# Kernel optimization log

Measured on AMD Instinct MI355X. Metric: run time of the kernel, lower is better.

The kernel has to match this reference:

```python
import jax, jax.numpy as jnp
import numpy as np

B, S, D, H, E = 4, 1024, 1024, 16, 4
HD = D // H
FF = 4 * D
EPS = 1e-5


def _ln(x):
    # normalize only; per-expert affine applied by caller
    mu = jnp.mean(x, axis=-1, keepdims=True)
    var = jnp.mean(jnp.square(x - mu), axis=-1, keepdims=True)
    return (x - mu) * jax.lax.rsqrt(var + EPS)


def setup_inputs() -> dict:
    key = jax.random.key(0)
    ks = jax.random.split(key, 12)
    s = 0.02
    inp = {
        "x": jax.random.normal(ks[0], (B, S, D), jnp.float32),
        # attention router
        "Wr_a": jax.random.normal(ks[1], (D, E), jnp.float32) * s,
        "br_a": jnp.zeros((E,), jnp.float32),
        # per-expert attention params
        "g_a": jnp.ones((E, D), jnp.float32),
        "b_a": jnp.zeros((E, D), jnp.float32),
        "Wqkv": jax.random.normal(ks[2], (E, D, 3 * D), jnp.float32) * s,
        "bqkv": jnp.zeros((E, 3 * D), jnp.float32),
        "Wpr": jax.random.normal(ks[3], (E, D, D), jnp.float32) * s,
        "bpr": jnp.zeros((E, D), jnp.float32),
        # MLP router
        "Wr_m": jax.random.normal(ks[4], (D, E), jnp.float32) * s,
        "br_m": jnp.zeros((E,), jnp.float32),
        # per-expert MLP params
        "g_m": jnp.ones((E, D), jnp.float32),
        "b_m": jnp.zeros((E, D), jnp.float32),
        "Wfc": jax.random.normal(ks[5], (E, D, FF), jnp.float32) * s,
        "bfc": jnp.zeros((E, FF), jnp.float32),
        "Wp2": jax.random.normal(ks[6], (E, FF, D), jnp.float32) * s,
        "bp2": jnp.zeros((E, D), jnp.float32),
    }
    return inp


def _block(x, Wr_a, br_a, g_a, b_a, Wqkv, bqkv, Wpr, bpr,
           Wr_m, br_m, g_m, b_m, Wfc, bfc, Wp2, bp2):
    N = B * S
    h = x.reshape(N, D)

    # ---- MoT attention (routing_all_possible_path: dense score-weighted mix) ----
    score = jax.nn.softmax(h @ Wr_a + br_a, axis=-1)          # [N,E]
    hn = _ln(h)                                                # shared normalization
    hln = hn[None, :, :] * g_a[:, None, :] + b_a[:, None, :]  # [E,N,D]
    qkv_e = jnp.einsum('end,edf->enf', hln, Wqkv) + bqkv[:, None, :]  # [E,N,3D]
    qkv = jnp.einsum('ne,enf->nf', score, qkv_e)               # [N,3D]

    q, k, v = jnp.split(qkv.reshape(B, S, 3 * D), 3, axis=-1)
    q = q.reshape(B, S, H, HD).transpose(0, 2, 1, 3)           # [B,H,S,hd]
    k = k.reshape(B, S, H, HD).transpose(0, 2, 1, 3)
    v = v.reshape(B, S, H, HD).transpose(0, 2, 1, 3)

    aw = jnp.einsum('bhqd,bhkd->bhqk', q, k) / jnp.sqrt(jnp.float32(HD))
    causal = jnp.tril(jnp.ones((S, S), bool))
    aw = jnp.where(causal, aw, jnp.finfo(aw.dtype).min)
    p = jax.nn.softmax(aw, axis=-1)
    a = jnp.einsum('bhqk,bhkd->bhqd', p, v)                    # [B,H,S,hd]
    a = a.transpose(0, 2, 1, 3).reshape(N, D)

    attn_out = jnp.einsum('ne,nd,edf->nf', score, a, Wpr) + score @ bpr
    y = x + attn_out.reshape(B, S, D)

    # ---- MoT MLP (same dense routed-expert pattern) ----
    h2 = y.reshape(N, D)
    score2 = jax.nn.softmax(h2 @ Wr_m + br_m, axis=-1)         # [N,E]
    hn2 = _ln(h2)
    hln2 = hn2[None, :, :] * g_m[:, None, :] + b_m[:, None, :]  # [E,N,D]
    inter = jax.nn.gelu(jnp.einsum('end,edf->enf', hln2, Wfc) + bfc[:, None, :])  # [E,N,FF]
    mlp_out = jnp.einsum('ne,enf,efd->nd', score2, inter, Wp2) + score2 @ bp2
    return y + mlp_out.reshape(B, S, D)


def reference(x, Wr_a, br_a, g_a, b_a, Wqkv, bqkv, Wpr, bpr,
              Wr_m, br_m, g_m, b_m, Wfc, bfc, Wp2, bp2):
    return _block(x, Wr_a, br_a, g_a, b_a, Wqkv, bqkv, Wpr, bpr,
                  Wr_m, br_m, g_m, b_m, Wfc, bfc, Wp2, bp2)
```

## Files before the change

### kernel.cpp

```cpp
#include <hip/hip_runtime.h>
#include <hip/hip_bf16.h>

typedef __bf16 bf16x8 __attribute__((ext_vector_type(8)));
typedef float f32x4 __attribute__((ext_vector_type(4)));
typedef unsigned short u16;
typedef u16 u16x8 __attribute__((ext_vector_type(8)));
typedef u16 u16x4 __attribute__((ext_vector_type(4)));

#define B_ 4
#define S_ 1024
#define D_ 1024
#define E_ 4
#define H_ 16
#define FF_ 4096
#define N_ 4096

__device__ __forceinline__ u16 f2bf(float f) {
  __hip_bfloat16 h = __float2bfloat16(f);
  return *reinterpret_cast<u16*>(&h);
}
__device__ __forceinline__ float bf2f(u16 v) {
  return __uint_as_float(((unsigned)v) << 16);
}

#define BAR()                         \
  {                                   \
    asm volatile("" ::: "memory");    \
    __builtin_amdgcn_s_barrier();     \
    asm volatile("" ::: "memory");    \
  }

__global__ __launch_bounds__(256) void tcvt(const float* __restrict__ src,
                                            u16* __restrict__ dst, int R, int C) {
  __shared__ float t[32][33];
  int r0 = blockIdx.y * 32, c0 = blockIdx.x * 32;
  int tx = threadIdx.x, ty = threadIdx.y;
#pragma unroll
  for (int i = 0; i < 4; i++)
    t[ty + i * 8][tx] = src[(long)(r0 + ty + i * 8) * C + c0 + tx];
  __syncthreads();
#pragma unroll
  for (int i = 0; i < 4; i++)
    dst[(long)(c0 + ty + i * 8) * R + r0 + tx] = f2bf(t[tx][ty + i * 8]);
}

template <int YMODE>
__global__ __launch_bounds__(256) void ln_router_expand(
    const float* __restrict__ X, const float* __restrict__ Wr, const float* __restrict__ br,
    const float* __restrict__ g, const float* __restrict__ bb,
    float* __restrict__ score_out, u16* __restrict__ Aout,
    long stride_e, long stride_n, int scale_flag,
    const float* __restrict__ score_a, const float* __restrict__ bpr,
    const u16* __restrict__ prt, float* __restrict__ ybuf) {
  int n = blockIdx.x, t = threadIdx.x;
  int lane = t & 63, wave = t >> 6;
  int d0 = t * 4;
  const float* xr = X + (long)n * D_;
  float4 xv = *reinterpret_cast<const float4*>(&xr[d0]);
  if (YMODE) {
    float4 sa4 = reinterpret_cast<const float4*>(score_a)[n];
    float4 b0 = *reinterpret_cast<const float4*>(&bpr[d0]);
    float4 b1 = *reinterpret_cast<const float4*>(&bpr[D_ + d0]);
    float4 b2 = *reinterpret_cast<const float4*>(&bpr[2 * D_ + d0]);
    float4 b3 = *reinterpret_cast<const float4*>(&bpr[3 * D_ + d0]);
    xv.x += sa4.x * b0.x + sa4.y * b1.x + sa4.z * b2.x + sa4.w * b3.x;
    xv.y += sa4.x * b0.y + sa4.y * b1.y + sa4.z * b2.y + sa4.w * b3.y;
    xv.z += sa4.x * b0.z + sa4.y * b1.z + sa4.z * b2.z + sa4.w * b3.z;
    xv.w += sa4.x * b0.w + sa4.y * b1.w + sa4.z * b2.w + sa4.w * b3.w;
    long idx = (long)n * D_ + d0;
#pragma unroll
    for (int zz = 0; zz < 4; zz++) {
      u16x4 pv = *reinterpret_cast<const u16x4*>(&prt[(long)zz * 4194304 + idx]);
      xv.x += bf2f(pv[0]); xv.y += bf2f(pv[1]); xv.z += bf2f(pv[2]); xv.w += bf2f(pv[3]);
    }
    *reinterpret_cast<float4*>(&ybuf[idx]) = xv;
  }
  float vals[6];
  vals[0] = xv.x + xv.y + xv.z + xv.w;
  vals[1] = xv.x * xv.x + xv.y * xv.y + xv.z * xv.z + xv.w * xv.w;
  {
    float4 w0 = reinterpret_cast<const float4*>(Wr)[d0];
    float4 w1 = reinterpret_cast<const float4*>(Wr)[d0 + 1];
    float4 w2 = reinterpret_cast<const float4*>(Wr)[d0 + 2];
    float4 w3 = reinterpret_cast<const float4*>(Wr)[d0 + 3];
    vals[2] = xv.x * w0.x + xv.y * w1.x + xv.z * w2.x + xv.w * w3.x;
    vals[3] = xv.x * w0.y + xv.y * w1.y + xv.z * w2.y + xv.w * w3.y;
    vals[4] = xv.x * w0.z + xv.y * w1.z + xv.z * w2.z + xv.w * w3.z;
    vals[5] = xv.x * w0.w + xv.y * w1.w + xv.z * w2.w + xv.w * w3.w;
  }
#pragma unroll
  for (int o = 1; o < 64; o <<= 1) {
#pragma unroll
    for (int j = 0; j < 6; j++) vals[j] += __shfl_xor(vals[j], o, 64);
  }
  __shared__ float red[4][6];
  if (lane == 0) {
#pragma unroll
    for (int j = 0; j < 6; j++) red[wave][j] = vals[j];
  }
  __syncthreads();
  float tot[6];
#pragma unroll
  for (int j = 0; j < 6; j++) tot[j] = red[0][j] + red[1][j] + red[2][j] + red[3][j];
  float mean = tot[0] * (1.0f / D_);
  float var = tot[1] * (1.0f / D_) - mean * mean;
  float rstd = rsqrtf(var + 1e-5f);
  float lg0 = tot[2] + br[0], lg1 = tot[3] + br[1], lg2 = tot[4] + br[2], lg3 = tot[5] + br[3];
  float mx = fmaxf(fmaxf(lg0, lg1), fmaxf(lg2, lg3));
  float e0 = __expf(lg0 - mx), e1 = __expf(lg1 - mx), e2 = __expf(lg2 - mx), e3 = __expf(lg3 - mx);
  float inv = 1.0f / (e0 + e1 + e2 + e3);
  float sc[4] = {e0 * inv, e1 * inv, e2 * inv, e3 * inv};
  if (t == 0) {
    float4 s4 = make_float4(sc[0], sc[1], sc[2], sc[3]);
    *reinterpret_cast<float4*>(&score_out[(long)n * 4]) = s4;
  }
  float4 hn;
  hn.x = (xv.x - mean) * rstd; hn.y = (xv.y - mean) * rstd;
  hn.z = (xv.z - mean) * rstd; hn.w = (xv.w - mean) * rstd;
#pragma unroll
  for (int e = 0; e < 4; e++) {
    float4 ge = *reinterpret_cast<const float4*>(&g[e * D_ + d0]);
    float4 be = *reinterpret_cast<const float4*>(&bb[e * D_ + d0]);
    float s = scale_flag ? sc[e] : 1.0f;
    u16x4 o;
    o[0] = f2bf((hn.x * ge.x + be.x) * s);
    o[1] = f2bf((hn.y * ge.y + be.y) * s);
    o[2] = f2bf((hn.z * ge.z + be.z) * s);
    o[3] = f2bf((hn.w * ge.w + be.w) * s);
    *reinterpret_cast<u16x4*>(&Aout[(long)e * stride_e + (long)n * stride_n + d0]) = o;
  }
}

template <int MODE>
__global__ __launch_bounds__(512, 2) void g8(
    const u16* __restrict__ A, const u16* __restrict__ Bt, int K, int N, int kslice,
    const float* __restrict__ score, const float* __restrict__ bias,
    u16* __restrict__ outb, int eidx, long zstride) {
  __shared__ __align__(16) u16 lds0[65536];
  const int tid = threadIdx.x;
  const int w = tid >> 6, lane = tid & 63;
  const int l15 = lane & 15, l4 = lane >> 4;
  const int wr = w >> 2, wc = w & 3;

  const int gx = gridDim.x, gy = gridDim.y;
  const int total = gx * gy * gridDim.z;
  const int flat = blockIdx.x + gx * (blockIdx.y + gy * blockIdx.z);
  const int cpx = total >> 3;
  const int nf = (flat & 7) * cpx + (flat >> 3);
  const int bxi = nf % gx;
  const int tmp = nf / gx;
  const int byi = tmp % gy;
  const int z = tmp / gy;

  const long bm = (long)byi * 256, bn = (long)bxi * 256;
  const long k0 = (long)z * kslice;
  const int nt = kslice >> 6;

  const int cp = lane & 3;
  const int sr0 = w * 32 + (lane >> 2);
  const int sr1 = sr0 + 16;
  const int cl0 = cp ^ ((sr0 >> 1) & 3);
  const int cl1 = cp ^ ((sr1 >> 1) & 3);
  const u16* gA0 = A + (bm + sr0) * (long)K + k0 + cl0 * 8;
  const u16* gA1 = A + (bm + sr1) * (long)K + k0 + cl1 * 8;
  const u16* gB0 = Bt + (bn + sr0) * (long)K + k0 + cl0 * 8;
  const u16* gB1 = Bt + (bn + sr1) * (long)K + k0 + cl1 * 8;
  const int e0 = w * 1024;
  const int e1 = w * 1024 + 512;

  const int chA = l4 ^ ((l15 >> 1) & 3);
  const int rdA = (wr * 128 + l15) * 32 + chA * 8;
  const int rdB = (wc * 64 + l15) * 32 + chA * 8;

#define GLD(gsrc, ldsoff)                                                              \
  __builtin_amdgcn_global_load_lds(                                                    \
      (const __attribute__((address_space(1))) void*)(gsrc),                           \
      (__attribute__((address_space(3))) void*)(lds0 + (ldsoff)), 16, 0, 0)

  GLD(gA0, 0 + e0);
  GLD(gA1, 0 + e1);
  GLD(gB0, 16384 + e0);
  GLD(gB1, 16384 + e1);
  GLD(gA0 + 32, 8192 + e0);
  GLD(gA1 + 32, 8192 + e1);
  GLD(gB0 + 32, 24576 + e0);
  GLD(gB1 + 32, 24576 + e1);
  if (nt > 1) {
    GLD(gA0 + 64, 32768 + e0);
    GLD(gA1 + 64, 32768 + e1);
    GLD(gB0 + 64, 32768 + 16384 + e0);
    GLD(gB1 + 64, 32768 + 16384 + e1);
    asm volatile("s_waitcnt vmcnt(8)" ::: "memory");
  } else {
    asm volatile("s_waitcnt vmcnt(4)" ::: "memory");
  }
  BAR();

  f32x4 acc[8][4] = {};
  bf16x8 a[8], b[4];

  for (int t = 0; t < nt; ++t) {
    const int base = (t & 1) * 32768;
    const int nb = base ^ 32768;
    const long ko1 = (long)(t + 1) * 64 + 32;
    const long ko2 = (long)(t + 2) * 64;
#pragma unroll
    for (int i = 0; i < 8; i++) a[i] = *(const bf16x8*)(lds0 + base + rdA + i * 512);
#pragma unroll
    for (int i = 0; i < 4; i++) b[i] = *(const bf16x8*)(lds0 + base + 16384 + rdB + i * 512);
    if (t + 1 < nt) {
      GLD(gA0 + ko1, nb + 8192 + e0);
      GLD(gA1 + ko1, nb + 8192 + e1);
      GLD(gB0 + ko1, nb + 24576 + e0);
      GLD(gB1 + ko1, nb + 24576 + e1);
    }
    BAR();
    __builtin_amdgcn_s_setprio(1);
#pragma unroll
    for (int mi = 0; mi < 8; mi++)
#pragma unroll
      for (int ni = 0; ni < 4; ni++)
        acc[mi][ni] = __builtin_amdgcn_mfma_f32_16x16x32_bf16(a[mi], b[ni], acc[mi][ni], 0, 0, 0);
    __builtin_amdgcn_s_setprio(0);
    if (t + 1 < nt) {
      asm volatile("s_waitcnt vmcnt(8)" ::: "memory");
    } else {
      asm volatile("s_waitcnt vmcnt(0)" ::: "memory");
    }
    BAR();
#pragma unroll
    for (int i = 0; i < 8; i++) a[i] = *(const bf16x8*)(lds0 + base + 8192 + rdA + i * 512);
#pragma unroll
    for (int i = 0; i < 4; i++) b[i] = *(const bf16x8*)(lds0 + base + 24576 + rdB + i * 512);
    if (t + 2 < nt) {
      GLD(gA0 + ko2, base + e0);
      GLD(gA1 + ko2, base + e1);
      GLD(gB0 + ko2, base + 16384 + e0);
      GLD(gB1 + ko2, base + 16384 + e1);
    }
    BAR();
    __builtin_amdgcn_s_setprio(1);
#pragma unroll
    for (int mi = 0; mi < 8; mi++)
#pragma unroll
      for (int ni = 0; ni < 4; ni++)
        acc[mi][ni] = __builtin_amdgcn_mfma_f32_16x16x32_bf16(a[mi], b[ni], acc[mi][ni], 0, 0, 0);
    __builtin_amdgcn_s_setprio(0);
    if (t + 2 < nt) {
      asm volatile("s_waitcnt vmcnt(8)" ::: "memory");
    } else if (t + 1 < nt) {
      asm volatile("s_waitcnt vmcnt(4)" ::: "memory");
    } else {
      asm volatile("s_waitcnt vmcnt(0)" ::: "memory");
    }
    BAR();
  }
#undef GLD

  const long zoff = (long)z * zstride;
#pragma unroll
  for (int ni = 0; ni < 4; ni++) {
    long col = bn + wc * 64 + ni * 16 + l15;
    float b4[4];
    float bcol = 0.0f;
    if (MODE == 0) {
#pragma unroll
      for (int e = 0; e < 4; e++) b4[e] = bias[(long)e * N + col];
    } else if (MODE == 2) {
      bcol = bias[col];
    }
#pragma unroll
    for (int mi = 0; mi < 8; mi++) {
#pragma unroll
      for (int r = 0; r < 4; r++) {
        long row = bm + wr * 128 + mi * 16 + l4 * 4 + r;
        float v = acc[mi][ni][r];
        if (MODE == 0) {
          float4 s4 = reinterpret_cast<const float4*>(score)[row];
          v += s4.x * b4[0] + s4.y * b4[1] + s4.z * b4[2] + s4.w * b4[3];
          outb[row * (long)N + col] = f2bf(v);
        } else if (MODE == 2) {
          float u = v + bcol;
          float zz = 0.7978845608f * (u + 0.044715f * u * u * u);
          float tt = __expf(2.0f * zz);
          float gel = u * (1.0f - 1.0f / (tt + 1.0f));
          outb[row * (long)N + col] = f2bf(gel * score[row * 4 + eidx]);
        } else {
          outb[zoff + row * (long)N + col] = f2bf(v);
        }
      }
    }
  }
}

__global__ __launch_bounds__(256) void attn_kernel(const u16* __restrict__ qkv,
                                                   const float* __restrict__ score_a,
                                                   u16* __restrict__ A_pr) {
  __shared__ __align__(16) u16 Kt[32 * 64];
  __shared__ __align__(16) u16 VT[64 * 32];
  __shared__ __align__(16) u16 Pl[4][16 * 32];
  int tid = threadIdx.x, wave = tid >> 6, lane = tid & 63;
  int l15 = lane & 15, l4 = lane >> 4;
  int qblk = blockIdx.x, bh = blockIdx.y;
  int b = bh >> 4, h = bh & 15;
  int q0 = qblk * 64 + wave * 16;
  const long LD = 3072;

  bf16x8 qf[2];
  {
    const u16* qp = qkv + (long)(b * 1024 + q0 + l15) * LD + h * 64 + l4 * 8;
    qf[0] = *(const bf16x8*)qp;
    qf[1] = *(const bf16x8*)(qp + 32);
  }
  f32x4 acc[4] = {};
  float m_run = -1e30f, l_run = 0.0f;
  int kv_end = qblk * 64 + 64;

  for (int kv0 = 0; kv0 < kv_end; kv0 += 32) {
    {
      int r = tid >> 3, c = (tid & 7) * 8;
      const u16* kp = qkv + (long)(b * 1024 + kv0 + r) * LD + 1024 + h * 64 + c;
      *(u16x8*)&Kt[r * 64 + c] = *(const u16x8*)kp;
      u16x8 vv = *(const u16x8*)(kp + 1024);
#pragma unroll
      for (int j = 0; j < 8; j++) VT[(c + j) * 32 + r] = vv[j];
    }
    __syncthreads();
    if (kv0 < q0 + 16) {
      float p[8];
      float pmax = -1e30f;
      int qg = q0 + l15;
#pragma unroll
      for (int ks = 0; ks < 2; ks++) {
        f32x4 st = {};
#pragma unroll
        for (int kc = 0; kc < 2; kc++) {
          bf16x8 kf = *(const bf16x8*)&Kt[(ks * 16 + l15) * 64 + kc * 32 + l4 * 8];
          st = __builtin_amdgcn_mfma_f32_16x16x32_bf16(kf, qf[kc], st, 0, 0, 0);
        }
#pragma unroll
        for (int r = 0; r < 4; r++) {
          int kvg = kv0 + ks * 16 + l4 * 4 + r;
          float v = st[r] * 0.125f;
          if (kvg > qg) v = -1e30f;
          p[ks * 4 + r] = v;
          pmax = fmaxf(pmax, v);
        }
      }
      pmax = fmaxf(pmax, __shfl_xor(pmax, 16, 64));
      pmax = fmaxf(pmax, __shfl_xor(pmax, 32, 64));
      float m_new = fmaxf(m_run, pmax);
      float alpha = __expf(m_run - m_new);
      float rsum = 0.f;
#pragma unroll
      for (int i = 0; i < 8; i++) {
        p[i] = __expf(p[i] - m_new);
        rsum += p[i];
      }
      rsum += __shfl_xor(rsum, 16, 64);
      rsum += __shfl_xor(rsum, 32, 64);
      l_run = l_run * alpha + rsum;
      m_run = m_new;
      float af4[4];
#pragma unroll
      for (int r = 0; r < 4; r++) af4[r] = __shfl(alpha, l4 * 4 + r, 64);
#pragma unroll
      for (int i = 0; i < 4; i++) {
#pragma unroll
        for (int r = 0; r < 4; r++) acc[i][r] *= af4[r];
      }
      u16* pw = &Pl[wave][0];
#pragma unroll
      for (int i = 0; i < 8; i++) {
        int ks = i >> 2, r = i & 3;
        pw[l15 * 32 + ks * 16 + l4 * 4 + r] = f2bf(p[i]);
      }
      bf16x8 pa = *(const bf16x8*)&pw[l15 * 32 + l4 * 8];
#pragma unroll
      for (int i = 0; i < 4; i++) {
        bf16x8 vf = *(const bf16x8*)&VT[(i * 16 + l15) * 32 + l4 * 8];
        acc[i] = __builtin_amdgcn_mfma_f32_16x16x32_bf16(pa, vf, acc[i], 0, 0, 0);
      }
    }
    __syncthreads();
  }

  float linv[4];
#pragma unroll
  for (int r = 0; r < 4; r++) {
    float lv = __shfl(l_run, l4 * 4 + r, 64);
    linv[r] = 1.0f / lv;
  }
#pragma unroll
  for (int r = 0; r < 4; r++) {
    int q = l4 * 4 + r;
    long nrow = (long)b * 1024 + q0 + q;
    float4 s4 = reinterpret_cast<const float4*>(score_a)[nrow];
    float se[4] = {s4.x, s4.y, s4.z, s4.w};
#pragma unroll
    for (int i = 0; i < 4; i++) {
      float v = acc[i][r] * linv[r];
      int d = h * 64 + i * 16 + l15;
#pragma unroll
      for (int e = 0; e < 4; e++) A_pr[nrow * 4096 + e * 1024 + d] = f2bf(se[e] * v);
    }
  }
}

template <int FIRST>
__global__ __launch_bounds__(256) void accum_out(const float* __restrict__ ybuf,
                                                 const float* __restrict__ score_m,
                                                 const float* __restrict__ bp2,
                                                 const u16* __restrict__ p2t,
                                                 float* __restrict__ out) {
  int n = blockIdx.x, t = threadIdx.x;
  int d0 = t * 4;
  long idx = (long)n * D_ + d0;
  float4 v;
  if (FIRST) {
    float4 s4 = reinterpret_cast<const float4*>(score_m)[n];
    float4 b0 = *reinterpret_cast<const float4*>(&bp2[d0]);
    float4 b1 = *reinterpret_cast<const float4*>(&bp2[D_ + d0]);
    float4 b2 = *reinterpret_cast<const float4*>(&bp2[2 * D_ + d0]);
    float4 b3 = *reinterpret_cast<const float4*>(&bp2[3 * D_ + d0]);
    v = *reinterpret_cast<const float4*>(&ybuf[idx]);
    v.x += s4.x * b0.x + s4.y * b1.x + s4.z * b2.x + s4.w * b3.x;
    v.y += s4.x * b0.y + s4.y * b1.y + s4.z * b2.y + s4.w * b3.y;
    v.z += s4.x * b0.z + s4.y * b1.z + s4.z * b2.z + s4.w * b3.z;
    v.w += s4.x * b0.w + s4.y * b1.w + s4.z * b2.w + s4.w * b3.w;
  } else {
    v = *reinterpret_cast<const float4*>(&out[idx]);
  }
#pragma unroll
  for (int zz = 0; zz < 4; zz++) {
    u16x4 pv = *reinterpret_cast<const u16x4*>(&p2t[(long)zz * 4194304 + idx]);
    v.x += bf2f(pv[0]); v.y += bf2f(pv[1]); v.z += bf2f(pv[2]); v.w += bf2f(pv[3]);
  }
  *reinterpret_cast<float4*>(&out[idx]) = v;
}

extern "C" void kernel_launch(void* const* d_in, const int* in_sizes, int n_in, void* d_out,
                              int out_size, void* d_ws, size_t ws_size, hipStream_t stream) {
  (void)in_sizes; (void)n_in; (void)out_size; (void)ws_size;
  const float* x    = (const float*)d_in[0];
  const float* Wr_a = (const float*)d_in[1];
  const float* br_a = (const float*)d_in[2];
  const float* g_a  = (const float*)d_in[3];
  const float* b_a  = (const float*)d_in[4];
  const float* Wqkv = (const float*)d_in[5];
  const float* bqkv = (const float*)d_in[6];
  const float* Wpr  = (const float*)d_in[7];
  const float* bpr  = (const float*)d_in[8];
  const float* Wr_m = (const float*)d_in[9];
  const float* br_m = (const float*)d_in[10];
  const float* g_m  = (const float*)d_in[11];
  const float* b_m  = (const float*)d_in[12];
  const float* Wfc  = (const float*)d_in[13];
  const float* bfc  = (const float*)d_in[14];
  const float* Wp2  = (const float*)d_in[15];
  const float* bp2  = (const float*)d_in[16];
  float* out = (float*)d_out;

  char* ws = (char*)d_ws;
  const size_t oW = 0;
  const size_t oA = 25165824;
  const size_t oQ = oA + 33554432;
  const size_t oP = oQ + 33554432;
  const size_t oY = oP + 33554432;
  const size_t oS = oY + 16777216;
  u16* wt_qkv  = (u16*)(ws + oW);
  u16* wt_pr   = (u16*)(ws + oW);
  u16* wt_fce  = (u16*)(ws + oW);
  u16* wt_p2e  = (u16*)(ws + oW + (size_t)8 * 1024 * 1024);
  u16* A_a     = (u16*)(ws + oA);
  u16* prt     = (u16*)(ws + oA);
  u16* A_fc    = (u16*)(ws + oA);
  u16* qkvb    = (u16*)(ws + oQ);
  u16* p2t     = (u16*)(ws + oQ);
  u16* A_pr    = (u16*)(ws + oP);
  u16* inter   = (u16*)(ws + oP);
  float* ybuf  = (float*)(ws + oY);
  float* score_a = (float*)(ws + oS);
  float* score_m = (float*)(ws + oS + 65536);

  dim3 tb(32, 8);
  tcvt<<<dim3(3072 / 32, 4096 / 32), tb, 0, stream>>>(Wqkv, wt_qkv, 4096, 3072);
  ln_router_expand<0><<<N_, 256, 0, stream>>>(x, Wr_a, br_a, g_a, b_a, score_a, A_a,
                                              (long)1024, (long)4096, 1,
                                              nullptr, nullptr, nullptr, nullptr);
  g8<0><<<dim3(3072 / 256, 4096 / 256, 1), 512, 0, stream>>>(
      A_a, wt_qkv, 4096, 3072, 4096, score_a, bqkv, qkvb, 0, 0L);
  attn_kernel<<<dim3(S_ / 64, B_ * H_), 256, 0, stream>>>(qkvb, score_a, A_pr);
  tcvt<<<dim3(1024 / 32, 4096 / 32), tb, 0, stream>>>(Wpr, wt_pr, 4096, 1024);
  g8<4><<<dim3(1024 / 256, 4096 / 256, 4), 512, 0, stream>>>(
      A_pr, wt_pr, 4096, 1024, 1024, nullptr, nullptr, prt, 0, (long)4096 * 1024);

  ln_router_expand<1><<<N_, 256, 0, stream>>>(x, Wr_m, br_m, g_m, b_m,
                                              score_m, A_fc, (long)N_ * 1024, (long)1024, 0,
                                              score_a, bpr, prt, ybuf);
  for (int e = 0; e < 4; e++) {
    tcvt<<<dim3(4096 / 32, 1024 / 32), tb, 0, stream>>>(
        Wfc + (size_t)e * 1024 * 4096, wt_fce, 1024, 4096);
    g8<2><<<dim3(4096 / 256, 4096 / 256, 1), 512, 0, stream>>>(
        A_fc + (size_t)e * N_ * 1024, wt_fce, 1024, 4096, 1024, score_m,
        bfc + e * 4096, inter, e, 0L);
    tcvt<<<dim3(1024 / 32, 4096 / 32), tb, 0, stream>>>(
        Wp2 + (size_t)e * 4096 * 1024, wt_p2e, 4096, 1024);
    g8<4><<<dim3(1024 / 256, 4096 / 256, 4), 512, 0, stream>>>(
        inter, wt_p2e, 4096, 1024, 1024, nullptr, nullptr, p2t, 0, (long)4096 * 1024);
    if (e == 0) {
      accum_out<1><<<N_, 256, 0, stream>>>(ybuf, score_m, bp2, p2t, out);
    } else {
      accum_out<0><<<N_, 256, 0, stream>>>(nullptr, nullptr, nullptr, p2t, out);
    }
  }
}
```

Measured before the change: 800.3 us.

## Double-buffer GEMM LDS fragments in registers to overlap reads with MFMA

Measured after the change: 789.4 us. No clear change (-1.4%).

```diff
diff --git a/kernel.cpp b/kernel.cpp
--- a/kernel.cpp
+++ b/kernel.cpp
@@ -190,68 +190,80 @@
     GLD(gA1 + 64, 32768 + e1);
     GLD(gB0 + 64, 32768 + 16384 + e0);
     GLD(gB1 + 64, 32768 + 16384 + e1);
+    GLD(gA0 + 96, 32768 + 8192 + e0);
+    GLD(gA1 + 96, 32768 + 8192 + e1);
+    GLD(gB0 + 96, 32768 + 24576 + e0);
+    GLD(gB1 + 96, 32768 + 24576 + e1);
     asm volatile("s_waitcnt vmcnt(8)" ::: "memory");
   } else {
-    asm volatile("s_waitcnt vmcnt(4)" ::: "memory");
+    asm volatile("s_waitcnt vmcnt(0)" ::: "memory");
   }
   BAR();
 
   f32x4 acc[8][4] = {};
-  bf16x8 a[8], b[4];
+  bf16x8 aC[8], bC[4], aN[8], bN[4];
+
+#pragma unroll
+  for (int i = 0; i < 8; i++) aC[i] = *(const bf16x8*)(lds0 + rdA + i * 512);
+#pragma unroll
+  for (int i = 0; i < 4; i++) bC[i] = *(const bf16x8*)(lds0 + 16384 + rdB + i * 512);
 
   for (int t = 0; t < nt; ++t) {
     const int base = (t & 1) * 32768;
     const int nb = base ^ 32768;
-    const long ko1 = (long)(t + 1) * 64 + 32;
     const long ko2 = (long)(t + 2) * 64;
 #pragma unroll
-    for (int i = 0; i < 8; i++) a[i] = *(const bf16x8*)(lds0 + base + rdA + i * 512);
-#pragma unroll
-    for (int i = 0; i < 4; i++) b[i] = *(const bf16x8*)(lds0 + base + 16384 + rdB + i * 512);
-    if (t + 1 < nt) {
-      GLD(gA0 + ko1, nb + 8192 + e0);
-      GLD(gA1 + ko1, nb + 8192 + e1);
-      GLD(gB0 + ko1, nb + 24576 + e0);
-      GLD(gB1 + ko1, nb + 24576 + e1);
-    }
-    BAR();
-    __builtin_amdgcn_s_setprio(1);
-#pragma unroll
-    for (int mi = 0; mi < 8; mi++)
-#pragma unroll
-      for (int ni = 0; ni < 4; ni++)
-        acc[mi][ni] = __builtin_amdgcn_mfma_f32_16x16x32_bf16(a[mi], b[ni], acc[mi][ni], 0, 0, 0);
-    __builtin_amdgcn_s_setprio(0);
-    if (t + 1 < nt) {
-      asm volatile("s_waitcnt vmcnt(8)" ::: "memory");
-    } else {
-      asm volatile("s_waitcnt vmcnt(0)" ::: "memory");
-    }
-    BAR();
-#pragma unroll
-    for (int i = 0; i < 8; i++) a[i] = *(const bf16x8*)(lds0 + base + 8192 + rdA + i * 512);
-#pragma unroll
-    for (int i = 0; i < 4; i++) b[i] = *(const bf16x8*)(lds0 + base + 24576 + rdB + i * 512);
+    for (int i = 0; i < 8; i++) aN[i] = *(const bf16x8*)(lds0 + base + 8192 + rdA + i * 512);
+#pragma unroll
+    for (int i = 0; i < 4; i++) bN[i] = *(const bf16x8*)(lds0 + base + 24576 + rdB + i * 512);
     if (t + 2 < nt) {
       GLD(gA0 + ko2, base + e0);
       GLD(gA1 + ko2, base + e1);
       GLD(gB0 + ko2, base + 16384 + e0);
       GLD(gB1 + ko2, base + 16384 + e1);
     }
+    __builtin_amdgcn_s_setprio(1);
+#pragma unroll
+    for (int mi = 0; mi < 8; mi++)
+#pragma unroll
+      for (int ni = 0; ni < 4; ni++)
+        acc[mi][ni] = __builtin_amdgcn_mfma_f32_16x16x32_bf16(aC[mi], bC[ni], acc[mi][ni], 0, 0, 0);
+    __builtin_amdgcn_s_setprio(0);
+    asm volatile("s_waitcnt lgkmcnt(0)" ::: "memory");
+    if (t + 1 < nt) {
+      if (t + 2 < nt) {
+        asm volatile("s_waitcnt vmcnt(8)" ::: "memory");
+      } else {
+        asm volatile("s_waitcnt vmcnt(4)" ::: "memory");
+      }
+    }
     BAR();
+    if (t + 1 < nt) {
+#pragma unroll
+      for (int i = 0; i < 8; i++) aC[i] = *(const bf16x8*)(lds0 + nb + rdA + i * 512);
+#pragma unroll
+      for (int i = 0; i < 4; i++) bC[i] = *(const bf16x8*)(lds0 + nb + 16384 + rdB + i * 512);
+    }
+    if (t + 2 < nt) {
+      GLD(gA0 + ko2 + 32, base + 8192 + e0);
+      GLD(gA1 + ko2 + 32, base + 8192 + e1);
+      GLD(gB0 + ko2 + 32, base + 24576 + e0);
+      GLD(gB1 + ko2 + 32, base + 24576 + e1);
+    }
     __builtin_amdgcn_s_setprio(1);
 #pragma unroll
     for (int mi = 0; mi < 8; mi++)
 #pragma unroll
       for (int ni = 0; ni < 4; ni++)
-        acc[mi][ni] = __builtin_amdgcn_mfma_f32_16x16x32_bf16(a[mi], b[ni], acc[mi][ni], 0, 0, 0);
+        acc[mi][ni] = __builtin_amdgcn_mfma_f32_16x16x32_bf16(aN[mi], bN[ni], acc[mi][ni], 0, 0, 0);
     __builtin_amdgcn_s_setprio(0);
-    if (t + 2 < nt) {
-      asm volatile("s_waitcnt vmcnt(8)" ::: "memory");
-    } else if (t + 1 < nt) {
-      asm volatile("s_waitcnt vmcnt(4)" ::: "memory");
-    } else {
-      asm volatile("s_waitcnt vmcnt(0)" ::: "memory");
+    asm volatile("s_waitcnt lgkmcnt(0)" ::: "memory");
+    if (t + 1 < nt) {
+      if (t + 2 < nt) {
+        asm volatile("s_waitcnt vmcnt(8)" ::: "memory");
+      } else {
+        asm volatile("s_waitcnt vmcnt(0)" ::: "memory");
+      }
     }
     BAR();
   }
```

## Replace pipelined 256x256 GEMM with simple single-buffered 128x128 GEMM

Applied to the files above, without the earlier changes.

New measurement: 943.7 us. 17.9% more time.

```diff
diff --git a/kernel.cpp b/kernel.cpp
--- a/kernel.cpp
+++ b/kernel.cpp
@@ -22,13 +22,6 @@
 __device__ __forceinline__ float bf2f(u16 v) {
   return __uint_as_float(((unsigned)v) << 16);
 }
-
-#define BAR()                         \
-  {                                   \
-    asm volatile("" ::: "memory");    \
-    __builtin_amdgcn_s_barrier();     \
-    asm volatile("" ::: "memory");    \
-  }
 
 __global__ __launch_bounds__(256) void tcvt(const float* __restrict__ src,
                                             u16* __restrict__ dst, int R, int C) {
@@ -132,15 +125,15 @@
 }
 
 template <int MODE>
-__global__ __launch_bounds__(512, 2) void g8(
+__global__ __launch_bounds__(256) void g4(
     const u16* __restrict__ A, const u16* __restrict__ Bt, int K, int N, int kslice,
     const float* __restrict__ score, const float* __restrict__ bias,
     u16* __restrict__ outb, int eidx, long zstride) {
-  __shared__ __align__(16) u16 lds0[65536];
+  __shared__ __align__(16) u16 lds0[16384];
   const int tid = threadIdx.x;
   const int w = tid >> 6, lane = tid & 63;
   const int l15 = lane & 15, l4 = lane >> 4;
-  const int wr = w >> 2, wc = w & 3;
+  const int wr = w >> 1, wc = w & 1;
 
   const int gx = gridDim.x, gy = gridDim.y;
   const int total = gx * gy * gridDim.z;
@@ -152,24 +145,24 @@
   const int byi = tmp % gy;
   const int z = tmp / gy;
 
-  const long bm = (long)byi * 256, bn = (long)bxi * 256;
+  const long bm = (long)byi * 128, bn = (long)bxi * 128;
   const long k0 = (long)z * kslice;
   const int nt = kslice >> 6;
 
   const int cp = lane & 3;
-  const int sr0 = w * 32 + (lane >> 2);
-  const int sr1 = sr0 + 16;
+  const int sr0 = w * 16 + (lane >> 2);
+  const int sr1 = sr0 + 64;
   const int cl0 = cp ^ ((sr0 >> 1) & 3);
   const int cl1 = cp ^ ((sr1 >> 1) & 3);
   const u16* gA0 = A + (bm + sr0) * (long)K + k0 + cl0 * 8;
   const u16* gA1 = A + (bm + sr1) * (long)K + k0 + cl1 * 8;
   const u16* gB0 = Bt + (bn + sr0) * (long)K + k0 + cl0 * 8;
   const u16* gB1 = Bt + (bn + sr1) * (long)K + k0 + cl1 * 8;
-  const int e0 = w * 1024;
-  const int e1 = w * 1024 + 512;
+  const int e0 = w * 512;
+  const int e1 = w * 512 + 2048;
 
   const int chA = l4 ^ ((l15 >> 1) & 3);
-  const int rdA = (wr * 128 + l15) * 32 + chA * 8;
+  const int rdA = (wr * 64 + l15) * 32 + chA * 8;
   const int rdB = (wc * 64 + l15) * 32 + chA * 8;
 
 #define GLD(gsrc, ldsoff)                                                              \
@@ -177,83 +170,36 @@
       (const __attribute__((address_space(1))) void*)(gsrc),                           \
       (__attribute__((address_space(3))) void*)(lds0 + (ldsoff)), 16, 0, 0)
 
-  GLD(gA0, 0 + e0);
-  GLD(gA1, 0 + e1);
-  GLD(gB0, 16384 + e0);
-  GLD(gB1, 16384 + e1);
-  GLD(gA0 + 32, 8192 + e0);
-  GLD(gA1 + 32, 8192 + e1);
-  GLD(gB0 + 32, 24576 + e0);
-  GLD(gB1 + 32, 24576 + e1);
-  if (nt > 1) {
-    GLD(gA0 + 64, 32768 + e0);
-    GLD(gA1 + 64, 32768 + e1);
-    GLD(gB0 + 64, 32768 + 16384 + e0);
-    GLD(gB1 + 64, 32768 + 16384 + e1);
-    asm volatile("s_waitcnt vmcnt(8)" ::: "memory");
-  } else {
-    asm volatile("s_waitcnt vmcnt(4)" ::: "memory");
-  }
-  BAR();
-
-  f32x4 acc[8][4] = {};
-  bf16x8 a[8], b[4];
+  f32x4 acc[4][4] = {};
 
   for (int t = 0; t < nt; ++t) {
-    const int base = (t & 1) * 32768;
-    const int nb = base ^ 32768;
-    const long ko1 = (long)(t + 1) * 64 + 32;
-    const long ko2 = (long)(t + 2) * 64;
-#pragma unroll
-    for (int i = 0; i < 8; i++) a[i] = *(const bf16x8*)(lds0 + base + rdA + i * 512);
-#pragma unroll
-    for (int i = 0; i < 4; i++) b[i] = *(const bf16x8*)(lds0 + base + 16384 + rdB + i * 512);
-    if (t + 1 < nt) {
-      GLD(gA0 + ko1, nb + 8192 + e0);
-      GLD(gA1 + ko1, nb + 8192 + e1);
-      GLD(gB0 + ko1, nb + 24576 + e0);
-      GLD(gB1 + ko1, nb + 24576 + e1);
-    }
-    BAR();
-    __builtin_amdgcn_s_setprio(1);
-#pragma unroll
-    for (int mi = 0; mi < 8; mi++)
+    const long ko = (long)t * 64;
+    GLD(gA0 + ko, 0 + e0);
+    GLD(gA1 + ko, 0 + e1);
+    GLD(gA0 + ko + 32, 4096 + e0);
+    GLD(gA1 + ko + 32, 4096 + e1);
+    GLD(gB0 + ko, 8192 + e0);
+    GLD(gB1 + ko, 8192 + e1);
+    GLD(gB0 + ko + 32, 12288 + e0);
+    GLD(gB1 + ko + 32, 12288 + e1);
+    __syncthreads();
+#pragma unroll
+    for (int kc = 0; kc < 2; kc++) {
+      bf16x8 af[4], bfr[4];
+#pragma unroll
+      for (int mi = 0; mi < 4; mi++)
+        af[mi] = *(const bf16x8*)(lds0 + kc * 4096 + rdA + mi * 512);
 #pragma unroll
       for (int ni = 0; ni < 4; ni++)
-        acc[mi][ni] = __builtin_amdgcn_mfma_f32_16x16x32_bf16(a[mi], b[ni], acc[mi][ni], 0, 0, 0);
-    __builtin_amdgcn_s_setprio(0);
-    if (t + 1 < nt) {
-      asm volatile("s_waitcnt vmcnt(8)" ::: "memory");
-    } else {
-      asm volatile("s_waitcnt vmcnt(0)" ::: "memory");
-    }
-    BAR();
-#pragma unroll
-    for (int i = 0; i < 8; i++) a[i] = *(const bf16x8*)(lds0 + base + 8192 + rdA + i * 512);
-#pragma unroll
-    for (int i = 0; i < 4; i++) b[i] = *(const bf16x8*)(lds0 + base + 24576 + rdB + i * 512);
-    if (t + 2 < nt) {
-      GLD(gA0 + ko2, base + e0);
-      GLD(gA1 + ko2, base + e1);
-      GLD(gB0 + ko2, base + 16384 + e0);
-      GLD(gB1 + ko2, base + 16384 + e1);
-    }
-    BAR();
-    __builtin_amdgcn_s_setprio(1);
-#pragma unroll
-    for (int mi = 0; mi < 8; mi++)
-#pragma unroll
-      for (int ni = 0; ni < 4; ni++)
-        acc[mi][ni] = __builtin_amdgcn_mfma_f32_16x16x32_bf16(a[mi], b[ni], acc[mi][ni], 0, 0, 0);
-    __builtin_amdgcn_s_setprio(0);
-    if (t + 2 < nt) {
-      asm volatile("s_waitcnt vmcnt(8)" ::: "memory");
-    } else if (t + 1 < nt) {
-      asm volatile("s_waitcnt vmcnt(4)" ::: "memory");
-    } else {
-      asm volatile("s_waitcnt vmcnt(0)" ::: "memory");
-    }
-    BAR();
+        bfr[ni] = *(const bf16x8*)(lds0 + 8192 + kc * 4096 + rdB + ni * 512);
+#pragma unroll
+      for (int mi = 0; mi < 4; mi++)
+#pragma unroll
+        for (int ni = 0; ni < 4; ni++)
+          acc[mi][ni] =
+              __builtin_amdgcn_mfma_f32_16x16x32_bf16(af[mi], bfr[ni], acc[mi][ni], 0, 0, 0);
+    }
+    __syncthreads();
   }
 #undef GLD
 
@@ -270,10 +216,10 @@
       bcol = bias[col];
     }
 #pragma unroll
-    for (int mi = 0; mi < 8; mi++) {
+    for (int mi = 0; mi < 4; mi++) {
 #pragma unroll
       for (int r = 0; r < 4; r++) {
-        long row = bm + wr * 128 + mi * 16 + l4 * 4 + r;
+        long row = bm + wr * 64 + mi * 16 + l4 * 4 + r;
         float v = acc[mi][ni][r];
         if (MODE == 0) {
           float4 s4 = reinterpret_cast<const float4*>(score)[row];
@@ -488,11 +434,11 @@
   ln_router_expand<0><<<N_, 256, 0, stream>>>(x, Wr_a, br_a, g_a, b_a, score_a, A_a,
                                               (long)1024, (long)4096, 1,
                                               nullptr, nullptr, nullptr, nullptr);
-  g8<0><<<dim3(3072 / 256, 4096 / 256, 1), 512, 0, stream>>>(
+  g4<0><<<dim3(3072 / 128, 4096 / 128, 1), 256, 0, stream>>>(
       A_a, wt_qkv, 4096, 3072, 4096, score_a, bqkv, qkvb, 0, 0L);
   attn_kernel<<<dim3(S_ / 64, B_ * H_), 256, 0, stream>>>(qkvb, score_a, A_pr);
   tcvt<<<dim3(1024 / 32, 4096 / 32), tb, 0, stream>>>(Wpr, wt_pr, 4096, 1024);
-  g8<4><<<dim3(1024 / 256, 4096 / 256, 4), 512, 0, stream>>>(
+  g4<4><<<dim3(1024 / 128, 4096 / 128, 4), 256, 0, stream>>>(
       A_pr, wt_pr, 4096, 1024, 1024, nullptr, nullptr, prt, 0, (long)4096 * 1024);
 
   ln_router_expand<1><<<N_, 256, 0, stream>>>(x, Wr_m, br_m, g_m, b_m,
@@ -501,12 +447,12 @@
   for (int e = 0; e < 4; e++) {
     tcvt<<<dim3(4096 / 32, 1024 / 32), tb, 0, stream>>>(
         Wfc + (size_t)e * 1024 * 4096, wt_fce, 1024, 4096);
-    g8<2><<<dim3(4096 / 256, 4096 / 256, 1), 512, 0, stream>>>(
+    g4<2><<<dim3(4096 / 128, 4096 / 128, 1), 256, 0, stream>>>(
         A_fc + (size_t)e * N_ * 1024, wt_fce, 1024, 4096, 1024, score_m,
         bfc + e * 4096, inter, e, 0L);
     tcvt<<<dim3(1024 / 32, 4096 / 32), tb, 0, stream>>>(
         Wp2 + (size_t)e * 4096 * 1024, wt_p2e, 4096, 1024);
-    g8<4><<<dim3(1024 / 256, 4096 / 256, 4), 512, 0, stream>>>(
+    g4<4><<<dim3(1024 / 128, 4096 / 128, 4), 256, 0, stream>>>(
         inter, wt_p2e, 4096, 1024, 1024, nullptr, nullptr, p2t, 0, (long)4096 * 1024);
     if (e == 0) {
       accum_out<1><<<N_, 256, 0, stream>>>(ybuf, score_m, bp2, p2t, out);
```
